# Optimization experiments

Hardware: AMD Instinct MI355X
Metric: run time of the kernel (lower is better)

The kernel has to match this reference:

```python
import jax, jax.numpy as jnp
import numpy as np

N_HEADS = 16
EMBD = 1024
D_HEAD = EMBD // N_HEADS

def setup_inputs() -> dict:
    key = jax.random.key(0)
    ks = jax.random.split(key, 5)
    x = jax.random.normal(ks[0], (2, 2048, EMBD), dtype=jnp.float32)
    # Linear weights stored torch-style [out, in]; apply as x @ W.T + b
    W_in = jax.random.normal(ks[1], (3 * EMBD, EMBD), dtype=jnp.float32) * (EMBD ** -0.5)
    b_in = jax.random.normal(ks[2], (3 * EMBD,), dtype=jnp.float32) * 0.01
    W_out = jax.random.normal(ks[3], (EMBD, EMBD), dtype=jnp.float32) * (EMBD ** -0.5)
    b_out = jax.random.normal(ks[4], (EMBD,), dtype=jnp.float32) * 0.01
    return {"x": x, "W_in": W_in, "b_in": b_in, "W_out": W_out, "b_out": b_out}

def reference(x, W_in, b_in, W_out, b_out):
    B, S, D = x.shape
    qkv = x @ W_in.T + b_in                      # [B, S, 3D]
    q, k, v = jnp.split(qkv, 3, axis=-1)
    def heads(t):
        return t.reshape(B, S, N_HEADS, D_HEAD).transpose(0, 2, 1, 3)  # [B,H,S,d]
    q, k, v = heads(q), heads(k), heads(v)
    scale = 1.0 / jnp.sqrt(jnp.float32(D_HEAD))
    scores = jnp.einsum('bhqd,bhkd->bhqk', q, k) * scale
    weights = jax.nn.softmax(scores, axis=-1)
    out = jnp.einsum('bhqk,bhkd->bhqd', weights, v)  # [B,H,S,d]
    out = out.transpose(0, 2, 1, 3).reshape(B, S, D)
    return out @ W_out.T + b_out
```

## Files before the change

kernel.cpp:

```cpp
#include <hip/hip_runtime.h>
#include <cstdint>

#define EMBD 1024
#define NH 16
#define DH 64
#define BB 2
#define SS 2048
#define M_TOT (BB*SS)
#define N_QKV (3*EMBD)

typedef __bf16 bf16_t;
typedef bf16_t bf16x8 __attribute__((ext_vector_type(8)));
typedef float f32x4 __attribute__((ext_vector_type(4)));
typedef unsigned short u16;
typedef unsigned int u32;

static __device__ __forceinline__ u16 f2bf(float f) {
    union { float f; unsigned u; } c; c.f = f;
    unsigned u = c.u;
    unsigned r = (u + 0x7FFFu + ((u >> 16) & 1u)) >> 16;
    return (u16)r;
}

#define GLDS16(gp, lp) \
    __builtin_amdgcn_global_load_lds((const __attribute__((address_space(1))) void*)(gp), \
                                     (__attribute__((address_space(3))) void*)(lp), 16, 0, 0)

#define NX8 (M_TOT * EMBD / 8)
#define NWI8 (N_QKV * EMBD / 8)
#define NWO8 (EMBD * EMBD / 8)
__global__ void cast_all(const float* __restrict__ x, const float* __restrict__ wi,
                         const float* __restrict__ wo, u16* __restrict__ xb,
                         u16* __restrict__ wib, u16* __restrict__ wob) {
    int i = blockIdx.x * blockDim.x + threadIdx.x;
    const float* s; u16* d; int off;
    if (i < NX8)              { s = x;  d = xb;  off = i; }
    else if (i < NX8 + NWI8)  { s = wi; d = wib; off = i - NX8; }
    else                      { s = wo; d = wob; off = i - NX8 - NWI8; }
    const float4* s4 = (const float4*)s;
    float4 a = s4[2 * off];
    float4 b = s4[2 * off + 1];
    union { u16 u[8]; uint4 v; } r;
    r.u[0] = f2bf(a.x); r.u[1] = f2bf(a.y); r.u[2] = f2bf(a.z); r.u[3] = f2bf(a.w);
    r.u[4] = f2bf(b.x); r.u[5] = f2bf(b.y); r.u[6] = f2bf(b.z); r.u[7] = f2bf(b.w);
    ((uint4*)d)[off] = r.v;
}

#define QSCALE (0.125f * 1.4426950408889634f)
__global__ __launch_bounds__(256) void gemm_qkv(
    const u16* __restrict__ Xb,
    const u16* __restrict__ Wb,
    const float* __restrict__ b_in,
    u16* __restrict__ Q, u16* __restrict__ Kf, u16* __restrict__ Vpf)
{
    __shared__ u16 AB[3][8192];
    const int t = threadIdx.x;
    const int lane = t & 63;
    const int wave = t >> 6;
    const int wm = wave >> 1, wn = wave & 1;
    const int quad = lane >> 4, l16 = lane & 15;
    const int m0 = blockIdx.y * 128, n0 = blockIdx.x * 128;

    const int s0i = t, s1i = 256 + t;
    const u16* ga0 = Xb + (size_t)(m0 + (s0i >> 2)) * EMBD + (s0i & 3) * 8;
    const u16* ga1 = Xb + (size_t)(m0 + (s1i >> 2)) * EMBD + (s1i & 3) * 8;
    const u16* gb0 = Wb + (size_t)(n0 + (s0i >> 2)) * EMBD + (s0i & 3) * 8;
    const u16* gb1 = Wb + (size_t)(n0 + (s1i >> 2)) * EMBD + (s1i & 3) * 8;

    f32x4 acc[4][4] = {};

#pragma unroll
    for (int p = 0; p < 2; ++p) {
        u16* buf = &AB[p][0];
        GLDS16(ga0 + p * 32, buf + s0i * 8);
        GLDS16(ga1 + p * 32, buf + s1i * 8);
        GLDS16(gb0 + p * 32, buf + 4096 + s0i * 8);
        GLDS16(gb1 + p * 32, buf + 4096 + s1i * 8);
    }

    int bi = 0;
    int bw = 2;
    for (int it = 0; it < EMBD / 32; ++it) {
        asm volatile("s_waitcnt vmcnt(4)" ::: "memory");
        __syncthreads();
        {
            int k0 = (it + 2) * 32;
            u16* buf = &AB[bw][0];
            GLDS16(ga0 + k0, buf + s0i * 8);
            GLDS16(ga1 + k0, buf + s1i * 8);
            GLDS16(gb0 + k0, buf + 4096 + s0i * 8);
            GLDS16(gb1 + k0, buf + 4096 + s1i * 8);
        }
        const u16* As = &AB[bi][0];
        const u16* Bs = &AB[bi][4096];
        bf16x8 af[4], bfr[4];
#pragma unroll
        for (int im = 0; im < 4; ++im)
            af[im] = *(const bf16x8*)(As + (wm * 64 + im * 16 + l16) * 32 + quad * 8);
#pragma unroll
        for (int in = 0; in < 4; ++in)
            bfr[in] = *(const bf16x8*)(Bs + (wn * 64 + in * 16 + l16) * 32 + quad * 8);
#pragma unroll
        for (int im = 0; im < 4; ++im)
#pragma unroll
            for (int in = 0; in < 4; ++in)
                acc[im][in] = __builtin_amdgcn_mfma_f32_16x16x32_bf16(
                    af[im], bfr[in], acc[im][in], 0, 0, 0);
        bi = (bi == 2) ? 0 : bi + 1;
        bw = (bw == 2) ? 0 : bw + 1;
    }

#pragma unroll
    for (int im = 0; im < 4; ++im) {
        int rbase = m0 + wm * 64 + im * 16 + quad * 4;
        int b = rbase >> 11, ss = rbase & (SS - 1);
#pragma unroll
        for (int in = 0; in < 4; ++in) {
            int col = n0 + wn * 64 + in * 16 + l16;
            float bias = b_in[col];
            float v0 = acc[im][in][0] + bias;
            float v1 = acc[im][in][1] + bias;
            float v2 = acc[im][in][2] + bias;
            float v3 = acc[im][in][3] + bias;
            if (col < EMBD) {
                int h = col >> 6, d = col & 63;
                u16* qp = Q + (((size_t)(b * NH + h) * SS) + ss) * DH + d;
                qp[0]      = f2bf(v0 * QSCALE);
                qp[DH]     = f2bf(v1 * QSCALE);
                qp[2 * DH] = f2bf(v2 * QSCALE);
                qp[3 * DH] = f2bf(v3 * QSCALE);
            } else if (col < 2 * EMBD) {
                int c = col - EMBD; int h = c >> 6, d = c & 63;
                int qf = (d >> 3) & 3;
                int sA = (ss >> 1) & 3;
                int sB = (sA + 1) & 3;
                u16* kp = Kf + (size_t)(b * NH + h) * SS * DH
                          + (ss >> 4) * 1024 + (d >> 5) * 512
                          + (ss & 15) * 32 + (d & 7);
                kp[(qf ^ sA) * 8]      = f2bf(v0);
                kp[32 + (qf ^ sA) * 8] = f2bf(v1);
                kp[64 + (qf ^ sB) * 8] = f2bf(v2);
                kp[96 + (qf ^ sB) * 8] = f2bf(v3);
            } else {
                int c = col - 2 * EMBD; int h = c >> 6, d = c & 63;
                int p32 = ((((ss >> 2) & 3) ^ ((d >> 1) & 3)) * 8)
                          + ((ss >> 4) & 1) * 4;
                u32 lo = (u32)f2bf(v0) | ((u32)f2bf(v1) << 16);
                u32 hi = (u32)f2bf(v2) | ((u32)f2bf(v3) << 16);
                uint2 pk; pk.x = lo; pk.y = hi;
                *(uint2*)(Vpf + (size_t)(b * NH + h) * SS * DH
                          + (ss >> 5) * 2048 + (d >> 4) * 512 + (d & 15) * 32 + p32) = pk;
            }
        }
    }
}

#define OST 72
#define NCH (SS / 64)
__global__ __launch_bounds__(256, 2) void attn(
    const u16* __restrict__ Q, const u16* __restrict__ Kf,
    const u16* __restrict__ Vpf, u16* __restrict__ AO)
{
    __shared__ u16 KV[3][8192];
    const int t = threadIdx.x;
    const int lane = t & 63, w = t >> 6;
    const int quad = lane >> 4, l16 = lane & 15;
    const int sq8 = (quad ^ ((l16 >> 1) & 3)) * 8;
    const int b0 = blockIdx.x;
    const int bh = (b0 & 7) * 4 + ((b0 >> 3) & 3);
    const int qt = b0 >> 5;
    const int q0 = qt * 128 + w * 32;

    const u16* Qh = Q + ((size_t)bh * SS + q0) * DH;
    const u16* Kh = Kf + (size_t)bh * SS * DH;
    const u16* Vh = Vpf + (size_t)bh * SS * DH;

    bf16x8 qb[2][2];
#pragma unroll
    for (int qi = 0; qi < 2; ++qi) {
        qb[qi][0] = *(const bf16x8*)(Qh + (qi * 16 + l16) * DH + quad * 8);
        qb[qi][1] = *(const bf16x8*)(Qh + (qi * 16 + l16) * DH + 32 + quad * 8);
    }

    union { u16 u[8]; bf16x8 b; } onesu;
#pragma unroll
    for (int j = 0; j < 8; ++j) onesu.u[j] = 0x3F80u;
    const bf16x8 ones = onesu.b;

    f32x4 o[2][4] = {};
    f32x4 ol[2] = {};

#pragma unroll
    for (int p = 0; p < 2; ++p) {
        GLDS16(Kh + p * 4096 + t * 8,        &KV[p][0] + t * 8);
        GLDS16(Kh + p * 4096 + 2048 + t * 8, &KV[p][0] + 2048 + t * 8);
        GLDS16(Vh + p * 4096 + t * 8,        &KV[p][4096] + t * 8);
        GLDS16(Vh + p * 4096 + 2048 + t * 8, &KV[p][4096] + 2048 + t * 8);
    }

    int bi = 0, bw = 2;
    for (int it = 0; it < NCH; ++it) {
        asm volatile("s_waitcnt vmcnt(4)" ::: "memory");
        __syncthreads();
        if (it < NCH - 1) {
            const u16* kc = Kh + (it + 2) * 4096;
            const u16* vc = Vh + (it + 2) * 4096;
            u16* kb = &KV[bw][0];
            u16* vb = &KV[bw][4096];
            GLDS16(kc + t * 8,        kb + t * 8);
            GLDS16(kc + 2048 + t * 8, kb + 2048 + t * 8);
            GLDS16(vc + t * 8,        vb + t * 8);
            GLDS16(vc + 2048 + t * 8, vb + 2048 + t * 8);
        }
        const u16* Kb = &KV[bi][0];
        const u16* Vb = &KV[bi][4096];
#pragma unroll
        for (int g = 0; g < 2; ++g) {
            bf16x8 ka00 = *(const bf16x8*)(Kb + (2 * g) * 1024 +       l16 * 32 + sq8);
            bf16x8 ka01 = *(const bf16x8*)(Kb + (2 * g) * 1024 + 512 + l16 * 32 + sq8);
            bf16x8 ka10 = *(const bf16x8*)(Kb + (2 * g + 1) * 1024 +       l16 * 32 + sq8);
            bf16x8 ka11 = *(const bf16x8*)(Kb + (2 * g + 1) * 1024 + 512 + l16 * 32 + sq8);
            bf16x8 va0 = *(const bf16x8*)(Vb + g * 2048 +        l16 * 32 + sq8);
            bf16x8 va1 = *(const bf16x8*)(Vb + g * 2048 + 512  + l16 * 32 + sq8);
            bf16x8 va2 = *(const bf16x8*)(Vb + g * 2048 + 1024 + l16 * 32 + sq8);
            bf16x8 va3 = *(const bf16x8*)(Vb + g * 2048 + 1536 + l16 * 32 + sq8);
            bf16x8 pb[2];
#pragma unroll
            for (int qi = 0; qi < 2; ++qi) {
                f32x4 z0 = {0.f, 0.f, 0.f, 0.f};
                f32x4 z1 = {0.f, 0.f, 0.f, 0.f};
                __builtin_amdgcn_s_setprio(1);
                z0 = __builtin_amdgcn_mfma_f32_16x16x32_bf16(ka00, qb[qi][0], z0, 0, 0, 0);
                z0 = __builtin_amdgcn_mfma_f32_16x16x32_bf16(ka01, qb[qi][1], z0, 0, 0, 0);
                z1 = __builtin_amdgcn_mfma_f32_16x16x32_bf16(ka10, qb[qi][0], z1, 0, 0, 0);
                z1 = __builtin_amdgcn_mfma_f32_16x16x32_bf16(ka11, qb[qi][1], z1, 0, 0, 0);
                __builtin_amdgcn_s_setprio(0);
                u32 ue[8];
#pragma unroll
                for (int j = 0; j < 4; ++j) {
                    float e0 = __builtin_amdgcn_exp2f(z0[j]);
                    float e1 = __builtin_amdgcn_exp2f(z1[j]);
                    union { float f; u32 v; } c0, c1;
                    c0.f = e0; c1.f = e1;
                    ue[j] = c0.v + 0x8000u;
                    ue[4 + j] = c1.v + 0x8000u;
                }
                union { uint4 u; bf16x8 b; } cv;
                cv.u.x = __builtin_amdgcn_perm(ue[1], ue[0], 0x07060302u);
                cv.u.y = __builtin_amdgcn_perm(ue[3], ue[2], 0x07060302u);
                cv.u.z = __builtin_amdgcn_perm(ue[5], ue[4], 0x07060302u);
                cv.u.w = __builtin_amdgcn_perm(ue[7], ue[6], 0x07060302u);
                pb[qi] = cv.b;
            }
            __builtin_amdgcn_s_setprio(1);
            o[0][0] = __builtin_amdgcn_mfma_f32_16x16x32_bf16(va0, pb[0], o[0][0], 0, 0, 0);
            o[0][1] = __builtin_amdgcn_mfma_f32_16x16x32_bf16(va1, pb[0], o[0][1], 0, 0, 0);
            o[0][2] = __builtin_amdgcn_mfma_f32_16x16x32_bf16(va2, pb[0], o[0][2], 0, 0, 0);
            o[0][3] = __builtin_amdgcn_mfma_f32_16x16x32_bf16(va3, pb[0], o[0][3], 0, 0, 0);
            ol[0]   = __builtin_amdgcn_mfma_f32_16x16x32_bf16(ones, pb[0], ol[0], 0, 0, 0);
            o[1][0] = __builtin_amdgcn_mfma_f32_16x16x32_bf16(va0, pb[1], o[1][0], 0, 0, 0);
            o[1][1] = __builtin_amdgcn_mfma_f32_16x16x32_bf16(va1, pb[1], o[1][1], 0, 0, 0);
            o[1][2] = __builtin_amdgcn_mfma_f32_16x16x32_bf16(va2, pb[1], o[1][2], 0, 0, 0);
            o[1][3] = __builtin_amdgcn_mfma_f32_16x16x32_bf16(va3, pb[1], o[1][3], 0, 0, 0);
            ol[1]   = __builtin_amdgcn_mfma_f32_16x16x32_bf16(ones, pb[1], ol[1], 0, 0, 0);
            __builtin_amdgcn_s_setprio(0);
        }
        bi = (bi == 2) ? 0 : bi + 1;
        bw = (bw == 2) ? 0 : bw + 1;
    }

    float rl[2];
    rl[0] = 1.0f / ol[0][0];
    rl[1] = 1.0f / ol[1][0];
    __syncthreads();
    u16* Ksc = &KV[0][0];
#pragma unroll
    for (int qi = 0; qi < 2; ++qi)
#pragma unroll
        for (int dt = 0; dt < 4; ++dt)
#pragma unroll
            for (int jj = 0; jj < 2; ++jj) {
                u32 lo_ = (u32)f2bf(o[qi][dt][2 * jj] * rl[qi]);
                u32 hi_ = (u32)f2bf(o[qi][dt][2 * jj + 1] * rl[qi]);
                *(u32*)(Ksc + (w * 32 + qi * 16 + l16) * OST + dt * 16 + quad * 4 + jj * 2) =
                    lo_ | (hi_ << 16);
            }
    __syncthreads();
    const int b = bh >> 4, h = bh & 15;
#pragma unroll
    for (int i = 0; i < 4; ++i) {
        int idx = i * 256 + t;
        int q = idx >> 3, c = idx & 7;
        uint4 vv = *(const uint4*)(Ksc + q * OST + c * 8);
        *(uint4*)(AO + ((size_t)(b * SS + qt * 128 + q)) * EMBD + h * DH + c * 8) = vv;
    }
}

__global__ __launch_bounds__(256) void gemm_out(
    const u16* __restrict__ Ab,
    const u16* __restrict__ Wb,
    const float* __restrict__ b_out,
    float* __restrict__ Out)
{
    __shared__ u16 AB[3][12288];
    const int t = threadIdx.x;
    const int lane = t & 63;
    const int wave = t >> 6;
    const int quad = lane >> 4, l16 = lane & 15;
    const int m0 = blockIdx.y * 128, n0 = blockIdx.x * 64;

    const int srow = t >> 3;
    const int scol = ((t & 7) ^ (srow & 7)) * 8;
    const u16* gaA[4];
#pragma unroll
    for (int i = 0; i < 4; ++i)
        gaA[i] = Ab + (size_t)(m0 + i * 32 + srow) * EMBD + scol;
    const u16* gbB[2];
#pragma unroll
    for (int i = 0; i < 2; ++i)
        gbB[i] = Wb + (size_t)(n0 + i * 32 + srow) * EMBD + scol;

    f32x4 acc[2][4] = {};

#pragma unroll
    for (int p = 0; p < 2; ++p) {
        u16* buf = &AB[p][0];
#pragma unroll
        for (int i = 0; i < 4; ++i)
            GLDS16(gaA[i] + p * 64, buf + i * 2048 + t * 8);
#pragma unroll
        for (int i = 0; i < 2; ++i)
            GLDS16(gbB[i] + p * 64, buf + 8192 + i * 2048 + t * 8);
    }

    int bi = 0, bw = 2;
    for (int it = 0; it < EMBD / 64; ++it) {
        asm volatile("s_waitcnt vmcnt(6)" ::: "memory");
        __syncthreads();
        {
            int k0 = (it + 2) * 64;
            u16* buf = &AB[bw][0];
#pragma unroll
            for (int i = 0; i < 4; ++i)
                GLDS16(gaA[i] + k0, buf + i * 2048 + t * 8);
#pragma unroll
            for (int i = 0; i < 2; ++i)
                GLDS16(gbB[i] + k0, buf + 8192 + i * 2048 + t * 8);
        }
        const u16* As = &AB[bi][0];
        const u16* Bs = &AB[bi][8192];
        bf16x8 af[2][2], bfr[4][2];
#pragma unroll
        for (int im = 0; im < 2; ++im)
#pragma unroll
            for (int kk = 0; kk < 2; ++kk)
                af[im][kk] = *(const bf16x8*)(As + (wave * 32 + im * 16 + l16) * 64
                                              + (((kk * 4 + quad) ^ (l16 & 7)) * 8));
#pragma unroll
        for (int in = 0; in < 4; ++in)
#pragma unroll
            for (int kk = 0; kk < 2; ++kk)
                bfr[in][kk] = *(const bf16x8*)(Bs + (in * 16 + l16) * 64
                                               + (((kk * 4 + quad) ^ (l16 & 7)) * 8));
#pragma unroll
        for (int im = 0; im < 2; ++im)
#pragma unroll
            for (int in = 0; in < 4; ++in)
#pragma unroll
                for (int kk = 0; kk < 2; ++kk)
                    acc[im][in] = __builtin_amdgcn_mfma_f32_16x16x32_bf16(
                        af[im][kk], bfr[in][kk], acc[im][in], 0, 0, 0);
        bi = (bi == 2) ? 0 : bi + 1;
        bw = (bw == 2) ? 0 : bw + 1;
    }

#pragma unroll
    for (int im = 0; im < 2; ++im) {
        int rbase = m0 + wave * 32 + im * 16 + quad * 4;
#pragma unroll
        for (int in = 0; in < 4; ++in) {
            int col = n0 + in * 16 + l16;
            float bias = b_out[col];
#pragma unroll
            for (int j = 0; j < 4; ++j)
                Out[(size_t)(rbase + j) * EMBD + col] = acc[im][in][j] + bias;
        }
    }
}

extern "C" void kernel_launch(void* const* d_in, const int* in_sizes, int n_in,
                              void* d_out, int out_size, void* d_ws, size_t ws_size,
                              hipStream_t stream)
{
    (void)in_sizes; (void)n_in; (void)out_size; (void)ws_size;
    const float* x     = (const float*)d_in[0];
    const float* W_in  = (const float*)d_in[1];
    const float* b_in  = (const float*)d_in[2];
    const float* W_out = (const float*)d_in[3];
    const float* b_out = (const float*)d_in[4];
    float* out = (float*)d_out;

    char* ws = (char*)d_ws;
    u16* xb  = (u16*)(ws);
    u16* wib = (u16*)(ws + 8u  * 1024 * 1024);
    u16* wob = (u16*)(ws + 14u * 1024 * 1024);
    u16* Qw  = (u16*)(ws + 16u * 1024 * 1024);
    u16* Kw  = (u16*)(ws + 24u * 1024 * 1024);
    u16* Vpw = (u16*)(ws + 32u * 1024 * 1024);
    u16* AO  = (u16*)(ws + 40u * 1024 * 1024);

    cast_all<<<(NX8 + NWI8 + NWO8) / 256, 256, 0, stream>>>(x, W_in, W_out, xb, wib, wob);
    gemm_qkv<<<dim3(N_QKV / 128, M_TOT / 128), 256, 0, stream>>>(xb, wib, b_in, Qw, Kw, Vpw);
    attn<<<512, 256, 0, stream>>>(Qw, Kw, Vpw, AO);
    gemm_out<<<dim3(EMBD / 64, M_TOT / 128), 256, 0, stream>>>(AO, wob, b_out, out);
}
```

Measured before the change: 176.2 us.

## Load V fragments straight to registers with double buffering, keep only K in LDS

V tiles no longer go through shared memory. Each lane loads its swizzled V fragments from global memory directly into registers, one iteration ahead, alternating between two register sets over a two-way unrolled loop. Only K goes through the LDS triple buffer, which halves LDS use. The S=QK^T MFMAs for both groups are batched ahead of the exp/PV stage. This removes LDS write/read traffic for V and frees shared memory, at the cost of more VGPRs (16 bf16x8 vectors), which may cause spills or lower occupancy. It also adds uncoalesced per-lane global loads for V, and the vmcnt waits now have to cover both direct loads and LDS DMA.

```diff
diff --git a/kernel.cpp b/kernel.cpp
--- a/kernel.cpp
+++ b/kernel.cpp
@@ -157,11 +157,93 @@
 
 #define OST 72
 #define NCH (SS / 64)
+
+#define ATTN_ITER(IT, VCUR, VNEXT)                                              \
+    {                                                                           \
+        const int it_ = (IT);                                                   \
+        if (it_ == NCH - 1) { asm volatile("s_waitcnt vmcnt(0)" ::: "memory"); }\
+        else                { asm volatile("s_waitcnt vmcnt(2)" ::: "memory"); }\
+        __syncthreads();                                                        \
+        if (it_ + 1 < NCH) {                                                    \
+            const u16* vsrc_ = vgl + (it_ + 1) * 4096;                          \
+            _Pragma("unroll")                                                   \
+            for (int g_ = 0; g_ < 2; ++g_)                                      \
+                _Pragma("unroll")                                               \
+                for (int r_ = 0; r_ < 4; ++r_)                                  \
+                    VNEXT[g_][r_] = *(const bf16x8*)(vsrc_ + g_ * 2048 + r_ * 512); \
+        }                                                                       \
+        if (it_ + 2 < NCH) {                                                    \
+            const u16* kc_ = Kh + (it_ + 2) * 4096;                             \
+            u16* kb_ = &KV[bw][0];                                              \
+            GLDS16(kc_ + t * 8,        kb_ + t * 8);                            \
+            GLDS16(kc_ + 2048 + t * 8, kb_ + 2048 + t * 8);                     \
+        }                                                                       \
+        const u16* Kb_ = &KV[bi][0];                                            \
+        bf16x8 ka_[2][4];                                                       \
+        _Pragma("unroll")                                                       \
+        for (int g_ = 0; g_ < 2; ++g_) {                                        \
+            ka_[g_][0] = *(const bf16x8*)(Kb_ + (2 * g_) * 1024 +       l16 * 32 + sq8); \
+            ka_[g_][1] = *(const bf16x8*)(Kb_ + (2 * g_) * 1024 + 512 + l16 * 32 + sq8); \
+            ka_[g_][2] = *(const bf16x8*)(Kb_ + (2 * g_ + 1) * 1024 +       l16 * 32 + sq8); \
+            ka_[g_][3] = *(const bf16x8*)(Kb_ + (2 * g_ + 1) * 1024 + 512 + l16 * 32 + sq8); \
+        }                                                                       \
+        f32x4 z_[2][2][2];                                                      \
+        __builtin_amdgcn_s_setprio(1);                                          \
+        _Pragma("unroll")                                                       \
+        for (int g_ = 0; g_ < 2; ++g_)                                          \
+            _Pragma("unroll")                                                   \
+            for (int qi_ = 0; qi_ < 2; ++qi_) {                                 \
+                f32x4 t0_ = {0.f, 0.f, 0.f, 0.f};                               \
+                f32x4 t1_ = {0.f, 0.f, 0.f, 0.f};                               \
+                t0_ = __builtin_amdgcn_mfma_f32_16x16x32_bf16(ka_[g_][0], qb[qi_][0], t0_, 0, 0, 0); \
+                t0_ = __builtin_amdgcn_mfma_f32_16x16x32_bf16(ka_[g_][1], qb[qi_][1], t0_, 0, 0, 0); \
+                t1_ = __builtin_amdgcn_mfma_f32_16x16x32_bf16(ka_[g_][2], qb[qi_][0], t1_, 0, 0, 0); \
+                t1_ = __builtin_amdgcn_mfma_f32_16x16x32_bf16(ka_[g_][3], qb[qi_][1], t1_, 0, 0, 0); \
+                z_[g_][qi_][0] = t0_; z_[g_][qi_][1] = t1_;                     \
+            }                                                                   \
+        __builtin_amdgcn_s_setprio(0);                                          \
+        _Pragma("unroll")                                                       \
+        for (int g_ = 0; g_ < 2; ++g_) {                                        \
+            bf16x8 pb_[2];                                                      \
+            _Pragma("unroll")                                                   \
+            for (int qi_ = 0; qi_ < 2; ++qi_) {                                 \
+                u32 ue_[8];                                                     \
+                _Pragma("unroll")                                               \
+                for (int j_ = 0; j_ < 4; ++j_) {                                \
+                    float e0_ = __builtin_amdgcn_exp2f(z_[g_][qi_][0][j_]);     \
+                    float e1_ = __builtin_amdgcn_exp2f(z_[g_][qi_][1][j_]);     \
+                    union { float f; u32 v; } c0_, c1_;                         \
+                    c0_.f = e0_; c1_.f = e1_;                                   \
+                    ue_[j_] = c0_.v + 0x8000u;                                  \
+                    ue_[4 + j_] = c1_.v + 0x8000u;                              \
+                }                                                               \
+                union { uint4 u; bf16x8 b; } cv_;                               \
+                cv_.u.x = __builtin_amdgcn_perm(ue_[1], ue_[0], 0x07060302u);   \
+                cv_.u.y = __builtin_amdgcn_perm(ue_[3], ue_[2], 0x07060302u);   \
+                cv_.u.z = __builtin_amdgcn_perm(ue_[5], ue_[4], 0x07060302u);   \
+                cv_.u.w = __builtin_amdgcn_perm(ue_[7], ue_[6], 0x07060302u);   \
+                pb_[qi_] = cv_.b;                                               \
+            }                                                                   \
+            __builtin_amdgcn_s_setprio(1);                                      \
+            o[0][0] = __builtin_amdgcn_mfma_f32_16x16x32_bf16(VCUR[g_][0], pb_[0], o[0][0], 0, 0, 0); \
+            o[0][1] = __builtin_amdgcn_mfma_f32_16x16x32_bf16(VCUR[g_][1], pb_[0], o[0][1], 0, 0, 0); \
+            o[0][2] = __builtin_amdgcn_mfma_f32_16x16x32_bf16(VCUR[g_][2], pb_[0], o[0][2], 0, 0, 0); \
+            o[0][3] = __builtin_amdgcn_mfma_f32_16x16x32_bf16(VCUR[g_][3], pb_[0], o[0][3], 0, 0, 0); \
+            ol[0]   = __builtin_amdgcn_mfma_f32_16x16x32_bf16(ones, pb_[0], ol[0], 0, 0, 0); \
+            o[1][0] = __builtin_amdgcn_mfma_f32_16x16x32_bf16(VCUR[g_][0], pb_[1], o[1][0], 0, 0, 0); \
+            o[1][1] = __builtin_amdgcn_mfma_f32_16x16x32_bf16(VCUR[g_][1], pb_[1], o[1][1], 0, 0, 0); \
+            o[1][2] = __builtin_amdgcn_mfma_f32_16x16x32_bf16(VCUR[g_][2], pb_[1], o[1][2], 0, 0, 0); \
+            o[1][3] = __builtin_amdgcn_mfma_f32_16x16x32_bf16(VCUR[g_][3], pb_[1], o[1][3], 0, 0, 0); \
+            ol[1]   = __builtin_amdgcn_mfma_f32_16x16x32_bf16(ones, pb_[1], ol[1], 0, 0, 0); \
+            __builtin_amdgcn_s_setprio(0);                                      \
+        }                                                                       \
+    }
+
 __global__ __launch_bounds__(256, 2) void attn(
     const u16* __restrict__ Q, const u16* __restrict__ Kf,
     const u16* __restrict__ Vpf, u16* __restrict__ AO)
 {
-    __shared__ u16 KV[3][8192];
+    __shared__ u16 KV[3][4096];
     const int t = threadIdx.x;
     const int lane = t & 63, w = t >> 6;
     const int quad = lane >> 4, l16 = lane & 15;
@@ -174,6 +256,7 @@
     const u16* Qh = Q + ((size_t)bh * SS + q0) * DH;
     const u16* Kh = Kf + (size_t)bh * SS * DH;
     const u16* Vh = Vpf + (size_t)bh * SS * DH;
+    const u16* vgl = Vh + l16 * 32 + sq8;
 
     bf16x8 qb[2][2];
 #pragma unroll
@@ -190,83 +273,24 @@
     f32x4 o[2][4] = {};
     f32x4 ol[2] = {};
 
+    bf16x8 vaA[2][4], vaB[2][4];
+#pragma unroll
+    for (int g = 0; g < 2; ++g)
+#pragma unroll
+        for (int r = 0; r < 4; ++r)
+            vaA[g][r] = *(const bf16x8*)(vgl + g * 2048 + r * 512);
 #pragma unroll
     for (int p = 0; p < 2; ++p) {
         GLDS16(Kh + p * 4096 + t * 8,        &KV[p][0] + t * 8);
         GLDS16(Kh + p * 4096 + 2048 + t * 8, &KV[p][0] + 2048 + t * 8);
-        GLDS16(Vh + p * 4096 + t * 8,        &KV[p][4096] + t * 8);
-        GLDS16(Vh + p * 4096 + 2048 + t * 8, &KV[p][4096] + 2048 + t * 8);
     }
 
     int bi = 0, bw = 2;
-    for (int it = 0; it < NCH; ++it) {
-        asm volatile("s_waitcnt vmcnt(4)" ::: "memory");
-        __syncthreads();
-        if (it < NCH - 1) {
-            const u16* kc = Kh + (it + 2) * 4096;
-            const u16* vc = Vh + (it + 2) * 4096;
-            u16* kb = &KV[bw][0];
-            u16* vb = &KV[bw][4096];
-            GLDS16(kc + t * 8,        kb + t * 8);
-            GLDS16(kc + 2048 + t * 8, kb + 2048 + t * 8);
-            GLDS16(vc + t * 8,        vb + t * 8);
-            GLDS16(vc + 2048 + t * 8, vb + 2048 + t * 8);
-        }
-        const u16* Kb = &KV[bi][0];
-        const u16* Vb = &KV[bi][4096];
-#pragma unroll
-        for (int g = 0; g < 2; ++g) {
-            bf16x8 ka00 = *(const bf16x8*)(Kb + (2 * g) * 1024 +       l16 * 32 + sq8);
-            bf16x8 ka01 = *(const bf16x8*)(Kb + (2 * g) * 1024 + 512 + l16 * 32 + sq8);
-            bf16x8 ka10 = *(const bf16x8*)(Kb + (2 * g + 1) * 1024 +       l16 * 32 + sq8);
-            bf16x8 ka11 = *(const bf16x8*)(Kb + (2 * g + 1) * 1024 + 512 + l16 * 32 + sq8);
-            bf16x8 va0 = *(const bf16x8*)(Vb + g * 2048 +        l16 * 32 + sq8);
-            bf16x8 va1 = *(const bf16x8*)(Vb + g * 2048 + 512  + l16 * 32 + sq8);
-            bf16x8 va2 = *(const bf16x8*)(Vb + g * 2048 + 1024 + l16 * 32 + sq8);
-            bf16x8 va3 = *(const bf16x8*)(Vb + g * 2048 + 1536 + l16 * 32 + sq8);
-            bf16x8 pb[2];
-#pragma unroll
-            for (int qi = 0; qi < 2; ++qi) {
-                f32x4 z0 = {0.f, 0.f, 0.f, 0.f};
-                f32x4 z1 = {0.f, 0.f, 0.f, 0.f};
-                __builtin_amdgcn_s_setprio(1);
-                z0 = __builtin_amdgcn_mfma_f32_16x16x32_bf16(ka00, qb[qi][0], z0, 0, 0, 0);
-                z0 = __builtin_amdgcn_mfma_f32_16x16x32_bf16(ka01, qb[qi][1], z0, 0, 0, 0);
-                z1 = __builtin_amdgcn_mfma_f32_16x16x32_bf16(ka10, qb[qi][0], z1, 0, 0, 0);
-                z1 = __builtin_amdgcn_mfma_f32_16x16x32_bf16(ka11, qb[qi][1], z1, 0, 0, 0);
-                __builtin_amdgcn_s_setprio(0);
-                u32 ue[8];
-#pragma unroll
-                for (int j = 0; j < 4; ++j) {
-                    float e0 = __builtin_amdgcn_exp2f(z0[j]);
-                    float e1 = __builtin_amdgcn_exp2f(z1[j]);
-                    union { float f; u32 v; } c0, c1;
-                    c0.f = e0; c1.f = e1;
-                    ue[j] = c0.v + 0x8000u;
-                    ue[4 + j] = c1.v + 0x8000u;
-                }
-                union { uint4 u; bf16x8 b; } cv;
-                cv.u.x = __builtin_amdgcn_perm(ue[1], ue[0], 0x07060302u);
-                cv.u.y = __builtin_amdgcn_perm(ue[3], ue[2], 0x07060302u);
-                cv.u.z = __builtin_amdgcn_perm(ue[5], ue[4], 0x07060302u);
-                cv.u.w = __builtin_amdgcn_perm(ue[7], ue[6], 0x07060302u);
-                pb[qi] = cv.b;
-            }
-            __builtin_amdgcn_s_setprio(1);
-            o[0][0] = __builtin_amdgcn_mfma_f32_16x16x32_bf16(va0, pb[0], o[0][0], 0, 0, 0);
-            o[0][1] = __builtin_amdgcn_mfma_f32_16x16x32_bf16(va1, pb[0], o[0][1], 0, 0, 0);
-            o[0][2] = __builtin_amdgcn_mfma_f32_16x16x32_bf16(va2, pb[0], o[0][2], 0, 0, 0);
-            o[0][3] = __builtin_amdgcn_mfma_f32_16x16x32_bf16(va3, pb[0], o[0][3], 0, 0, 0);
-            ol[0]   = __builtin_amdgcn_mfma_f32_16x16x32_bf16(ones, pb[0], ol[0], 0, 0, 0);
-            o[1][0] = __builtin_amdgcn_mfma_f32_16x16x32_bf16(va0, pb[1], o[1][0], 0, 0, 0);
-            o[1][1] = __builtin_amdgcn_mfma_f32_16x16x32_bf16(va1, pb[1], o[1][1], 0, 0, 0);
-            o[1][2] = __builtin_amdgcn_mfma_f32_16x16x32_bf16(va2, pb[1], o[1][2], 0, 0, 0);
-            o[1][3] = __builtin_amdgcn_mfma_f32_16x16x32_bf16(va3, pb[1], o[1][3], 0, 0, 0);
-            ol[1]   = __builtin_amdgcn_mfma_f32_16x16x32_bf16(ones, pb[1], ol[1], 0, 0, 0);
-            __builtin_amdgcn_s_setprio(0);
-        }
-        bi = (bi == 2) ? 0 : bi + 1;
-        bw = (bw == 2) ? 0 : bw + 1;
+    for (int it2 = 0; it2 < NCH; it2 += 2) {
+        ATTN_ITER(it2, vaA, vaB);
+        bi = (bi == 2) ? 0 : bi + 1; bw = (bw == 2) ? 0 : bw + 1;
+        ATTN_ITER(it2 + 1, vaB, vaA);
+        bi = (bi == 2) ? 0 : bi + 1; bw = (bw == 2) ? 0 : bw + 1;
     }
 
     float rl[2];
```

Result: no change. 177.6 us (+0.8%).
